# Kernel tuning notes

Hardware: AMD Instinct MI355X
Metric: run time of the kernel (lower is better)

Reference implementation:

```python
import jax, jax.numpy as jnp
import numpy as np

N_NODES = 50000
N_EDGES = 800000
N_REL = 16
N_GRAPHS = 64
IN_DIM = 128
HID = 128
FC = 256
N_CLASSES = 16


def setup_inputs() -> dict:
    key = jax.random.key(0)
    ks = jax.random.split(key, 16)
    h = jax.random.normal(ks[0], (N_NODES, IN_DIM), dtype=jnp.float32)
    src = jax.random.randint(ks[1], (N_EDGES,), 0, N_NODES, dtype=jnp.int32)
    dst = jax.random.randint(ks[2], (N_EDGES,), 0, N_NODES, dtype=jnp.int32)
    rel_types = jax.random.randint(ks[3], (N_EDGES,), 0, N_REL, dtype=jnp.int32)
    graph_ids = jnp.sort(jax.random.randint(ks[4], (N_NODES,), 0, N_GRAPHS, dtype=jnp.int32))
    s1 = 1.0 / np.sqrt(IN_DIM)
    s2 = 1.0 / np.sqrt(HID)
    # RGCN layer 1: per-relation weights, self-loop weight, bias
    W1 = jax.random.normal(ks[5], (N_REL, IN_DIM, HID), dtype=jnp.float32) * s1
    Ws1 = jax.random.normal(ks[6], (IN_DIM, HID), dtype=jnp.float32) * s1
    b1 = jnp.zeros((HID,), dtype=jnp.float32)
    # RGCN layer 2
    W2 = jax.random.normal(ks[7], (N_REL, HID, HID), dtype=jnp.float32) * s2
    Ws2 = jax.random.normal(ks[8], (HID, HID), dtype=jnp.float32) * s2
    b2 = jnp.zeros((HID,), dtype=jnp.float32)
    # FC layer after mean pooling
    Wfc = jax.random.normal(ks[9], (HID, FC), dtype=jnp.float32) * s2
    bfc = jnp.zeros((FC,), dtype=jnp.float32)
    # classify head
    Wc = jax.random.normal(ks[10], (FC, N_CLASSES), dtype=jnp.float32) * (1.0 / np.sqrt(FC))
    bc = jnp.zeros((N_CLASSES,), dtype=jnp.float32)
    return dict(h=h, src=src, dst=dst, rel_types=rel_types, graph_ids=graph_ids,
                W1=W1, Ws1=Ws1, b1=b1, W2=W2, Ws2=Ws2, b2=b2,
                Wfc=Wfc, bfc=bfc, Wc=Wc, bc=bc)


def _rel_graph_conv(h, W, Ws, b, src, dst, rel):
    # dgl RelGraphConv (regularizer=None, self_loop=True, bias=True):
    # out[v] = sum_{e:(u->v)} W[rel_e] @ h[u] + Ws @ h[v] + b
    hW = jnp.einsum('ni,rio->rno', h, W)            # [R, N, out]
    msg = hW[rel, src]                               # [E, out] gather per edge
    agg = jax.ops.segment_sum(msg, dst, num_segments=N_NODES)
    return agg + h @ Ws + b


def _mean_nodes(h, graph_ids):
    sums = jax.ops.segment_sum(h, graph_ids, num_segments=N_GRAPHS)      # [G, D]
    cnts = jax.ops.segment_sum(jnp.ones((h.shape[0], 1), h.dtype), graph_ids,
                               num_segments=N_GRAPHS)                    # [G, 1]
    return sums / jnp.maximum(cnts, 1.0)


def reference(h, src, dst, rel_types, graph_ids,
              W1, Ws1, b1, W2, Ws2, b2, Wfc, bfc, Wc, bc):
    h = h.astype(jnp.float32)
    h = jax.nn.relu(_rel_graph_conv(h, W1, Ws1, b1, src, dst, rel_types))
    h = jax.nn.relu(_rel_graph_conv(h, W2, Ws2, b2, src, dst, rel_types))
    hg = _mean_nodes(h, graph_ids)                   # [G, HID]
    hg = jax.nn.relu(hg @ Wfc + bfc)                 # [G, FC]
    return jax.nn.softmax(hg @ Wc + bc, axis=1)      # [G, n_classes]
```

## Files before the change

### kernel.cpp

```cpp
#include <hip/hip_runtime.h>
#include <hip/hip_bf16.h>

#define N_NODES   50000
#define N_PAD     50048
#define N_EDGES   800000
#define N_REL     16
#define N_GRAPHS  64
#define DIM       128
#define FC_DIM    256
#define N_CLASSES 16

#define SB        50176
#define NBINS_P   (16 * SB)
#define NBLK_PP   784
#define NCOARSE   782
#define NCH       98
#define CHSZ      8192
#define POOL_CH   64
#define NBVIRT    13328

#define WS_MARK   0
#define WS_HG     802816
#define WS_CNT    835584
#define WS_SRCOF  835840
#define MEMSET_SZ 4038912
#define WS_BLKH   4038912
#define WS_COFS   4345600
#define WS_PARTP  4348928
#define WS_BLKB   4352256
#define WS_RELB   4355584
#define WS_CIDMAP 4355840
#define WS_RTMP   7567104
#define WS_RECS   10767104
#define WS_OFFSD  13967104
#define WS_X1     14167552
#define WS_X2     26979840
#define WS_AGG    39792128
#define WS_WB     52604416
#define WS_T      53718528

#define XW_TOTAL  (N_PAD * DIM + 2 * 17 * 16384)

typedef __attribute__((ext_vector_type(8))) short bf16x8;
typedef __attribute__((ext_vector_type(4))) float f32x4;

__device__ __forceinline__ void atomAddF(float* p, float v) {
#if defined(__gfx90a__) || defined(__gfx942__) || defined(__gfx950__)
    unsafeAtomicAdd(p, v);
#else
    atomicAdd(p, v);
#endif
}

__device__ __forceinline__ float bf2f(unsigned int u) {
    union { float f; unsigned int i; } x; x.i = u << 16; return x.f;
}
__device__ __forceinline__ unsigned short f2bf(float f) {
    union { float f; unsigned int u; } x; x.f = f;
    unsigned int r = x.u + 0x7fff + ((x.u >> 16) & 1);
    return (unsigned short)(r >> 16);
}
__device__ __forceinline__ void accum8(float* qa, uint4 u) {
    qa[0] += bf2f(u.x & 0xffff); qa[1] += bf2f(u.x >> 16);
    qa[2] += bf2f(u.y & 0xffff); qa[3] += bf2f(u.y >> 16);
    qa[4] += bf2f(u.z & 0xffff); qa[5] += bf2f(u.z >> 16);
    qa[6] += bf2f(u.w & 0xffff); qa[7] += bf2f(u.w >> 16);
}
__device__ __forceinline__ void pack16(const float* qa, unsigned short* dst) {
    #pragma unroll
    for (int j = 0; j < 2; ++j) {
        uint4 w;
        w.x = ((unsigned int)f2bf(qa[j*8+1]) << 16) | f2bf(qa[j*8+0]);
        w.y = ((unsigned int)f2bf(qa[j*8+3]) << 16) | f2bf(qa[j*8+2]);
        w.z = ((unsigned int)f2bf(qa[j*8+5]) << 16) | f2bf(qa[j*8+4]);
        w.w = ((unsigned int)f2bf(qa[j*8+7]) << 16) | f2bf(qa[j*8+6]);
        ((uint4*)dst)[j] = w;
    }
}

__global__ void k_convXW(const float* __restrict__ h, unsigned short* __restrict__ x1,
                         const float* __restrict__ W1, const float* __restrict__ Ws1,
                         const float* __restrict__ W2, const float* __restrict__ Ws2,
                         unsigned short* __restrict__ Wb) {
    int id = blockIdx.x * blockDim.x + threadIdx.x;
    if (id < N_PAD * DIM) {
        int v = id >> 7;
        x1[id] = (v < N_NODES) ? f2bf(h[id]) : (unsigned short)0;
    } else {
        int t = id - N_PAD * DIM;
        int l = t / 278528, rem = t % 278528;
        int r = rem >> 14, rr = rem & 16383;
        int n = rr >> 7, k = rr & 127;
        const float* W  = l ? W2 : W1;
        const float* Ws = l ? Ws2 : Ws1;
        float v = (r < 16) ? W[r * 16384 + k * 128 + n] : Ws[k * 128 + n];
        Wb[t] = f2bf(v);
    }
}

__global__ __launch_bounds__(256) void k_h1(
    const int* __restrict__ src, const int* __restrict__ dst, const int* __restrict__ rel,
    unsigned char* __restrict__ mark, int* __restrict__ blockHist)
{
    __shared__ int hl[NCOARSE];
    int b = blockIdx.x, t = threadIdx.x;
    for (int i = t; i < NCOARSE; i += 256) hl[i] = 0;
    __syncthreads();
    int e0 = b * CHSZ;
    int eend = min(e0 + CHSZ, N_EDGES);
    for (int e = e0 + t; e < eend; e += 256) {
        int d = dst[e];
        mark[rel[e] * SB + src[e]] = 1;
        atomicAdd(&hl[d >> 6], 1);
    }
    __syncthreads();
    for (int i = t; i < NCOARSE; i += 256) blockHist[b * NCOARSE + i] = hl[i];
}

__global__ void k_cscan(int* __restrict__ blockHist, int* __restrict__ coarseOffs) {
    __shared__ int s1[1024], s2[1024];
    int t = threadIdx.x;
    int tot = 0;
    if (t < NCOARSE) {
        int run = 0;
        for (int b = 0; b < NCH; ++b) {
            int v = blockHist[b * NCOARSE + t];
            blockHist[b * NCOARSE + t] = run;
            run += v;
        }
        tot = run;
    }
    s1[t] = tot; __syncthreads();
    int* cur = s1; int* nxt = s2;
    for (int o = 1; o < 1024; o <<= 1) {
        nxt[t] = cur[t] + ((t >= o) ? cur[t - o] : 0);
        __syncthreads();
        int* tmp = cur; cur = nxt; nxt = tmp;
    }
    if (t < NCOARSE) {
        int base = cur[t] - tot;
        coarseOffs[t] = base;
        for (int b = 0; b < NCH; ++b) blockHist[b * NCOARSE + t] += base;
    }
    if (t == NCOARSE) coarseOffs[NCOARSE] = cur[NCOARSE - 1];
}

__global__ void k_scanPA(const unsigned int* __restrict__ markU, int* __restrict__ partP) {
    __shared__ int red[256];
    int b = blockIdx.x, t = threadIdx.x;
    unsigned int u = markU[b * 256 + t];
    red[t] = (int)((u & 1) + ((u >> 8) & 1) + ((u >> 16) & 1) + ((u >> 24) & 1));
    __syncthreads();
    for (int o = 128; o > 0; o >>= 1) {
        if (t < o) red[t] += red[t + o];
        __syncthreads();
    }
    if (t == 0) partP[b] = red[0];
}

__global__ void k_scanPB(const int* __restrict__ partP, int* __restrict__ blkB,
                         int* __restrict__ relB) {
    __shared__ int s1[784], s2[784];
    __shared__ int tot[16], rbase[17];
    int t = threadIdx.x;
    int rel = t / 49, pos = t - rel * 49;
    int v = (t < 784) ? partP[t] : 0;
    if (t < 784) s1[t] = v;
    __syncthreads();
    int* cur = s1; int* nxt = s2;
    for (int o = 1; o < 64; o <<= 1) {
        if (t < 784) nxt[t] = cur[t] + ((pos >= o) ? cur[t - o] : 0);
        __syncthreads();
        int* tmp = cur; cur = nxt; nxt = tmp;
    }
    if (t < 784 && pos == 48) tot[rel] = cur[t];
    __syncthreads();
    if (t == 0) {
        int base = 0;
        for (int r = 0; r < 16; ++r) { rbase[r] = base; base += (tot[r] + 63) & ~63; }
        rbase[16] = base;
    }
    __syncthreads();
    if (t < 784) blkB[t] = rbase[rel] + cur[t] - v;
    if (t < 17)  relB[t] = rbase[t];
}

__global__ void k_scanPC(const unsigned int* __restrict__ markU, const int* __restrict__ blkB,
                         int* __restrict__ cidMap, int* __restrict__ srcOf) {
    __shared__ int s1[256], s2[256];
    int b = blockIdx.x, t = threadIdx.x;
    unsigned int u = markU[b * 256 + t];
    int f0 = (int)(u & 1), f1 = (int)((u >> 8) & 1);
    int f2 = (int)((u >> 16) & 1), f3 = (int)((u >> 24) & 1);
    int sum = f0 + f1 + f2 + f3;
    s1[t] = sum; __syncthreads();
    int* cur = s1; int* nxt = s2;
    for (int o = 1; o < 256; o <<= 1) {
        nxt[t] = cur[t] + ((t >= o) ? cur[t - o] : 0);
        __syncthreads();
        int* tmp = cur; cur = nxt; nxt = tmp;
    }
    int cid = blkB[b] + cur[t] - sum;
    int rel = b / 49;
    int key0 = b * 1024 + t * 4;
    int srcBase = key0 - rel * SB;
    if (f0) { cidMap[key0]     = cid; srcOf[cid] = srcBase;     cid++; }
    if (f1) { cidMap[key0 + 1] = cid; srcOf[cid] = srcBase + 1; cid++; }
    if (f2) { cidMap[key0 + 2] = cid; srcOf[cid] = srcBase + 2; cid++; }
    if (f3) { cidMap[key0 + 3] = cid; srcOf[cid] = srcBase + 3; cid++; }
}

__global__ __launch_bounds__(256) void k_scat1(
    const int* __restrict__ src, const int* __restrict__ dst, const int* __restrict__ rel,
    const int* __restrict__ cidMap, const int* __restrict__ blockHist,
    unsigned int* __restrict__ rtmp)
{
    __shared__ int baseL[NCOARSE];
    __shared__ int hl[NCOARSE];
    int b = blockIdx.x, t = threadIdx.x;
    for (int i = t; i < NCOARSE; i += 256) { baseL[i] = blockHist[b * NCOARSE + i]; hl[i] = 0; }
    __syncthreads();
    int e0 = b * CHSZ;
    int eend = min(e0 + CHSZ, N_EDGES);
    for (int e = e0 + t; e < eend; e += 256) {
        int d = dst[e];
        int cid = cidMap[rel[e] * SB + src[e]];
        int c = d >> 6;
        int rank = atomicAdd(&hl[c], 1);
        rtmp[baseL[c] + rank] = ((unsigned int)cid << 6) | (unsigned int)(d & 63);
    }
}

__global__ __launch_bounds__(256) void k_p2(
    const unsigned int* __restrict__ rtmp, const int* __restrict__ coarseOffs,
    unsigned int* __restrict__ recs, int* __restrict__ offsD)
{
    __shared__ int cntL[64], exclL[65], cur2[64];
    int i = blockIdx.x, t = threadIdx.x;
    int segB = coarseOffs[i], segE = coarseOffs[i + 1];
    if (t < 64) { cntL[t] = 0; cur2[t] = 0; }
    __syncthreads();
    for (int e = segB + t; e < segE; e += 256)
        atomicAdd(&cntL[rtmp[e] & 63u], 1);
    __syncthreads();
    if (t == 0) {
        int run = segB;
        #pragma unroll
        for (int d = 0; d < 64; ++d) { exclL[d] = run; run += cntL[d]; }
        exclL[64] = run;
    }
    __syncthreads();
    if (t < 64) offsD[i * 64 + t] = exclL[t];
    if (t == 64) offsD[i * 64 + 64] = exclL[64];
    for (int e = segB + t; e < segE; e += 256) {
        unsigned int r = rtmp[e];
        int d = (int)(r & 63u);
        int rank = atomicAdd(&cur2[d], 1);
        recs[exclL[d] + rank] = r >> 6;
    }
}

__global__ __launch_bounds__(256) void k_phaseA(
    const unsigned short* __restrict__ x, const unsigned short* __restrict__ Wb,
    const int* __restrict__ srcOf, const int* __restrict__ relB,
    unsigned short* __restrict__ T)
{
    __shared__ unsigned short Xs[64 * 136];
    __shared__ unsigned short Cs[64 * 136];
    __shared__ int sSrc[64];
    __shared__ int sRB[17];

    int tid = threadIdx.x;
    if (tid < 17) sRB[tid] = relB[tid];
    __syncthreads();
    int rtot = sRB[16];

    for (int vb = blockIdx.x; vb < NBVIRT; vb += gridDim.x) {
        int chunk = vb / 136;
        int lane  = vb - chunk * 136;
        int r = lane >> 3;
        int i = chunk * 8 + (lane & 7);
        int base, cnt;
        if (r == 16) { base = rtot;    cnt = N_PAD / 64; }
        else         { base = sRB[r];  cnt = (sRB[r + 1] - base) >> 6; }
        if (i >= cnt) continue;
        int row0 = base + i * 64;

        __syncthreads();
        if (tid < 64) sSrc[tid] = (r == 16) ? (i * 64 + tid) : srcOf[row0 + tid];
        __syncthreads();

        {
            int row = tid >> 2, c0 = tid & 3;
            const uint4* xp = (const uint4*)(x + (size_t)sSrc[row] * DIM);
            uint4* lp = (uint4*)(&Xs[row * 136]);
            #pragma unroll
            for (int ii = 0; ii < 4; ++ii) lp[c0 + 4 * ii] = xp[c0 + 4 * ii];
        }
        __syncthreads();

        int w = tid >> 6, l = tid & 63;
        int nl = l & 15, q = l >> 4;

        bf16x8 Bf[2][4];
        const unsigned short* wr = Wb + r * 16384;
        #pragma unroll
        for (int nt = 0; nt < 2; ++nt) {
            int n = w * 32 + nt * 16 + nl;
            #pragma unroll
            for (int kc = 0; kc < 4; ++kc)
                Bf[nt][kc] = *(const bf16x8*)(wr + n * 128 + kc * 32 + q * 8);
        }
        #pragma unroll
        for (int m = 0; m < 4; ++m) {
            f32x4 a0 = {0.f,0.f,0.f,0.f}, a1 = {0.f,0.f,0.f,0.f};
            #pragma unroll
            for (int kc = 0; kc < 4; ++kc) {
                bf16x8 a = *(const bf16x8*)(&Xs[(m * 16 + nl) * 136 + kc * 32 + q * 8]);
                a0 = __builtin_amdgcn_mfma_f32_16x16x32_bf16(a, Bf[0][kc], a0, 0, 0, 0);
                a1 = __builtin_amdgcn_mfma_f32_16x16x32_bf16(a, Bf[1][kc], a1, 0, 0, 0);
            }
            int col = w * 32 + nl;
            #pragma unroll
            for (int reg = 0; reg < 4; ++reg) {
                int row = m * 16 + q * 4 + reg;
                Cs[row * 136 + col]      = f2bf(a0[reg]);
                Cs[row * 136 + col + 16] = f2bf(a1[reg]);
            }
        }
        __syncthreads();
        {
            unsigned short* Tb = T + (size_t)row0 * DIM;
            #pragma unroll
            for (int it = 0; it < 4; ++it) {
                int c = tid + it * 256;
                int row = c >> 4, k8 = c & 15;
                uint4 vv = *(const uint4*)(&Cs[row * 136 + k8 * 8]);
                *(uint4*)(Tb + row * DIM + k8 * 8) = vv;
            }
        }
    }
}

__global__ __launch_bounds__(256) void k_phaseB(
    const unsigned short* __restrict__ T, const unsigned int* __restrict__ recs,
    const int* __restrict__ offsD, const int* __restrict__ relB,
    const float* __restrict__ bias,
    unsigned short* __restrict__ aggOut, int relu)
{
    __shared__ int sOffs[33];
    __shared__ float sBias[128];
    __shared__ int sSelf;
    int tid = threadIdx.x;
    int v0 = blockIdx.x * 32;
    if (tid < 33) sOffs[tid] = offsD[v0 + tid];
    if (tid == 40) sSelf = relB[16];
    if (tid >= 64 && tid < 96) ((float4*)sBias)[tid - 64] = ((const float4*)bias)[tid - 64];
    __syncthreads();

    int g = tid >> 3, s = tid & 7;
    int dst = v0 + g;
    float qa[16];
    #pragma unroll
    for (int i = 0; i < 16; ++i) qa[i] = sBias[s * 16 + i];

    int beg = sOffs[g], end = sOffs[g + 1];
    int e = beg;
    for (; e + 3 < end; e += 4) {
        unsigned int c0 = recs[e], c1 = recs[e+1], c2 = recs[e+2], c3 = recs[e+3];
        const uint4* t0 = (const uint4*)(T + (size_t)c0 * DIM + s * 16);
        const uint4* t1 = (const uint4*)(T + (size_t)c1 * DIM + s * 16);
        const uint4* t2 = (const uint4*)(T + (size_t)c2 * DIM + s * 16);
        const uint4* t3 = (const uint4*)(T + (size_t)c3 * DIM + s * 16);
        uint4 a0 = t0[0], a1 = t0[1], b0 = t1[0], b1 = t1[1];
        uint4 cc0 = t2[0], cc1 = t2[1], d0 = t3[0], d1 = t3[1];
        accum8(qa, a0); accum8(qa + 8, a1);
        accum8(qa, b0); accum8(qa + 8, b1);
        accum8(qa, cc0); accum8(qa + 8, cc1);
        accum8(qa, d0); accum8(qa + 8, d1);
    }
    for (; e < end; ++e) {
        unsigned int c = recs[e];
        const uint4* tp = (const uint4*)(T + (size_t)c * DIM + s * 16);
        uint4 u0 = tp[0], u1 = tp[1];
        accum8(qa, u0); accum8(qa + 8, u1);
    }
    {
        const uint4* tp = (const uint4*)(T + (size_t)(sSelf + dst) * DIM + s * 16);
        uint4 u0 = tp[0], u1 = tp[1];
        accum8(qa, u0); accum8(qa + 8, u1);
    }

    if (relu) {
        #pragma unroll
        for (int i = 0; i < 16; ++i) qa[i] = fmaxf(qa[i], 0.f);
    }
    pack16(qa, aggOut + (size_t)dst * DIM + s * 16);
}

__global__ void k_pool(const unsigned short* __restrict__ agg2, const int* __restrict__ gids,
                       float* __restrict__ hg_sum, int* __restrict__ cnt)
{
    int d  = threadIdx.x;
    int n0 = blockIdx.x * POOL_CH;
    int nend = min(n0 + POOL_CH, N_NODES);
    if (n0 >= N_NODES) return;
    int curg = gids[n0];
    float run = 0.f;
    for (int n = n0; n < nend; ++n) {
        int g = gids[n];
        if (g != curg) { atomAddF(&hg_sum[curg*DIM + d], run); run = 0.f; curg = g; }
        run += fmaxf(bf2f((unsigned int)agg2[n*DIM + d]), 0.f);
    }
    atomAddF(&hg_sum[curg*DIM + d], run);
    if (d == 0) {
        int cg = gids[n0]; int rl = 0;
        for (int n = n0; n < nend; ++n) {
            int g = gids[n];
            if (g != cg) { atomicAdd(&cnt[cg], rl); rl = 0; cg = g; }
            rl++;
        }
        atomicAdd(&cnt[cg], rl);
    }
}

__global__ __launch_bounds__(256) void k_head(
    const float* __restrict__ hg_sum, const int* __restrict__ cnt,
    const float* __restrict__ Wfc, const float* __restrict__ bfc,
    const float* __restrict__ Wc, const float* __restrict__ bc,
    float* __restrict__ out)
{
    int g = blockIdx.x, t = threadIdx.x;
    __shared__ float hgl[DIM];
    __shared__ float fcl[FC_DIM];
    __shared__ float lg[N_CLASSES];
    if (t < DIM) {
        float c = (float)max(cnt[g], 1);
        hgl[t] = hg_sum[g*DIM + t] / c;
    }
    __syncthreads();
    {
        float sv = bfc[t];
        #pragma unroll 4
        for (int k = 0; k < DIM; ++k) sv += hgl[k] * Wfc[k*FC_DIM + t];
        fcl[t] = fmaxf(sv, 0.f);
    }
    __syncthreads();
    if (t < N_CLASSES) {
        float lgt = bc[t];
        #pragma unroll 4
        for (int k = 0; k < FC_DIM; ++k) lgt += fcl[k] * Wc[k*N_CLASSES + t];
        lg[t] = lgt;
    }
    __syncthreads();
    if (t < N_CLASSES) {
        float m = lg[0];
        #pragma unroll
        for (int c = 1; c < N_CLASSES; ++c) m = fmaxf(m, lg[c]);
        float sden = 0.f;
        #pragma unroll
        for (int c = 0; c < N_CLASSES; ++c) sden += expf(lg[c] - m);
        out[g*N_CLASSES + t] = expf(lg[t] - m) / sden;
    }
}

extern "C" void kernel_launch(void* const* d_in, const int* in_sizes, int n_in,
                              void* d_out, int out_size, void* d_ws, size_t ws_size,
                              hipStream_t stream)
{
    const float* h   = (const float*)d_in[0];
    const int*   src = (const int*)d_in[1];
    const int*   dst = (const int*)d_in[2];
    const int*   rel = (const int*)d_in[3];
    const int*   gid = (const int*)d_in[4];
    const float* W1  = (const float*)d_in[5];
    const float* Ws1 = (const float*)d_in[6];
    const float* b1  = (const float*)d_in[7];
    const float* W2  = (const float*)d_in[8];
    const float* Ws2 = (const float*)d_in[9];
    const float* b2  = (const float*)d_in[10];
    const float* Wfc = (const float*)d_in[11];
    const float* bfc = (const float*)d_in[12];
    const float* Wc  = (const float*)d_in[13];
    const float* bc  = (const float*)d_in[14];
    float* out = (float*)d_out;

    char* ws = (char*)d_ws;
    unsigned char* mark = (unsigned char*)(ws + WS_MARK);
    float* hgsum = (float*)(ws + WS_HG);
    int*   cnt   = (int*)(ws + WS_CNT);
    int*   srcOf = (int*)(ws + WS_SRCOF);
    int*   blkH  = (int*)(ws + WS_BLKH);
    int*   cOffs = (int*)(ws + WS_COFS);
    int*   partP = (int*)(ws + WS_PARTP);
    int*   blkB  = (int*)(ws + WS_BLKB);
    int*   relB  = (int*)(ws + WS_RELB);
    int*   cidMap= (int*)(ws + WS_CIDMAP);
    unsigned int* rtmp = (unsigned int*)(ws + WS_RTMP);
    unsigned int* recs = (unsigned int*)(ws + WS_RECS);
    int*   offsD = (int*)(ws + WS_OFFSD);
    unsigned short* x1  = (unsigned short*)(ws + WS_X1);
    unsigned short* x2  = (unsigned short*)(ws + WS_X2);
    unsigned short* agg = (unsigned short*)(ws + WS_AGG);
    unsigned short* Wb  = (unsigned short*)(ws + WS_WB);
    unsigned short* T   = (unsigned short*)(ws + WS_T);

    int gridA = NBVIRT;
    if (ws_size > (size_t)WS_T) {
        long long capRows = (long long)((ws_size - WS_T) / 256);
        long long capBlk = capRows / 64;
        if (capBlk < gridA) gridA = (int)capBlk;
    }

    hipMemsetAsync(mark, 0, MEMSET_SZ, stream);

    k_convXW<<<XW_TOTAL / 256, 256, 0, stream>>>(h, x1, W1, Ws1, W2, Ws2, Wb);
    k_h1<<<NCH, 256, 0, stream>>>(src, dst, rel, mark, blkH);

    k_cscan<<<1, 1024, 0, stream>>>(blkH, cOffs);
    k_scanPA<<<NBLK_PP, 256, 0, stream>>>((const unsigned int*)mark, partP);
    k_scanPB<<<1, 1024, 0, stream>>>(partP, blkB, relB);
    k_scanPC<<<NBLK_PP, 256, 0, stream>>>((const unsigned int*)mark, blkB, cidMap, srcOf);

    k_scat1<<<NCH, 256, 0, stream>>>(src, dst, rel, cidMap, blkH, rtmp);
    k_p2<<<NCOARSE, 256, 0, stream>>>(rtmp, cOffs, recs, offsD);

    k_phaseA<<<gridA, 256, 0, stream>>>(x1, Wb, srcOf, relB, T);
    k_phaseB<<<N_PAD / 32, 256, 0, stream>>>(T, recs, offsD, relB, b1, x2, 1);
    k_phaseA<<<gridA, 256, 0, stream>>>(x2, Wb + 17 * 16384, srcOf, relB, T);
    k_phaseB<<<N_PAD / 32, 256, 0, stream>>>(T, recs, offsD, relB, b2, agg, 0);

    k_pool<<<(N_PAD + POOL_CH - 1) / POOL_CH, 128, 0, stream>>>(agg, gid, hgsum, cnt);
    k_head<<<N_GRAPHS, 256, 0, stream>>>(hgsum, cnt, Wfc, bfc, Wc, bc, out);
}
```

Measured before the change: 439.8 us.

## Software-pipeline phaseA gathers with persistent grid and swizzled LDS output

Turns k_phaseA into a persistent kernel with a fixed grid of 1024 blocks. Each block prefetches the next tile's gathered source rows into registers while computing the current tile's MFMA, and no longer stages source indices in shared memory. It also XOR-swizzles the Cs staging buffer to reduce LDS bank conflicts. The intent is to hide gather latency and cut syncs per tile, at the cost of extra registers and dropping the workspace-capacity-based grid limit.

Result: no change. 433.9 us (-1.3%).

```diff
diff --git a/kernel.cpp b/kernel.cpp
--- a/kernel.cpp
+++ b/kernel.cpp
@@ -18,6 +18,7 @@
 #define CHSZ      8192
 #define POOL_CH   64
 #define NBVIRT    13328
+#define GRID_A    1024
 
 #define WS_MARK   0
 #define WS_HG     802816
@@ -265,9 +266,8 @@
     const int* __restrict__ srcOf, const int* __restrict__ relB,
     unsigned short* __restrict__ T)
 {
-    __shared__ unsigned short Xs[64 * 136];
-    __shared__ unsigned short Cs[64 * 136];
-    __shared__ int sSrc[64];
+    __shared__ __attribute__((aligned(16))) unsigned short Xs[64 * 136];
+    __shared__ __attribute__((aligned(16))) unsigned short Cs[64 * 136];
     __shared__ int sRB[17];
 
     int tid = threadIdx.x;
@@ -275,70 +275,94 @@
     __syncthreads();
     int rtot = sRB[16];
 
-    for (int vb = blockIdx.x; vb < NBVIRT; vb += gridDim.x) {
+    int row = tid >> 2, c0 = tid & 3;
+
+    auto tileInfo = [&](int vb, int& trow0, int& tr) -> bool {
         int chunk = vb / 136;
-        int lane  = vb - chunk * 136;
+        int lane = vb - chunk * 136;
         int r = lane >> 3;
         int i = chunk * 8 + (lane & 7);
         int base, cnt;
-        if (r == 16) { base = rtot;    cnt = N_PAD / 64; }
-        else         { base = sRB[r];  cnt = (sRB[r + 1] - base) >> 6; }
-        if (i >= cnt) continue;
-        int row0 = base + i * 64;
-
+        if (r == 16) { base = rtot; cnt = N_PAD / 64; }
+        else         { base = sRB[r]; cnt = (sRB[r + 1] - base) >> 6; }
+        if (i >= cnt) return false;
+        trow0 = base + i * 64; tr = r;
+        return true;
+    };
+
+    int vb = blockIdx.x;
+    int cur_row0, cur_r;
+    while (vb < NBVIRT && !tileInfo(vb, cur_row0, cur_r)) vb += gridDim.x;
+    if (vb >= NBVIRT) return;
+
+    uint4 g0, g1, g2, g3;
+    {
+        int sr = (cur_r == 16) ? (cur_row0 - rtot + row) : srcOf[cur_row0 + row];
+        const uint4* xp = (const uint4*)(x + (size_t)sr * DIM);
+        g0 = xp[c0]; g1 = xp[c0 + 4]; g2 = xp[c0 + 8]; g3 = xp[c0 + 12];
+    }
+
+    int w = tid >> 6, l = tid & 63;
+    int nl = l & 15, q = l >> 4;
+
+    while (true) {
+        {
+            uint4* lp = (uint4*)(&Xs[row * 136]);
+            lp[c0] = g0; lp[c0 + 4] = g1; lp[c0 + 8] = g2; lp[c0 + 12] = g3;
+        }
+        bf16x8 Bf[2][4];
+        {
+            const unsigned short* wr = Wb + cur_r * 16384;
+            #pragma unroll
+            for (int nt = 0; nt < 2; ++nt) {
+                int n = w * 32 + nt * 16 + nl;
+                #pragma unroll
+                for (int kc = 0; kc < 4; ++kc)
+                    Bf[nt][kc] = *(const bf16x8*)(wr + n * 128 + kc * 32 + q * 8);
+            }
+        }
+        int nvb = vb + gridDim.x;
+        int nxt_row0 = 0, nxt_r = 0;
+        while (nvb < NBVIRT && !tileInfo(nvb, nxt_row0, nxt_r)) nvb += gridDim.x;
+        bool nhave = (nvb < NBVIRT);
+        if (nhave) {
+            int sr = (nxt_r == 16) ? (nxt_row0 - rtot + row) : srcOf[nxt_row0 + row];
+            const uint4* xp = (const uint4*)(x + (size_t)sr * DIM);
+            g0 = xp[c0]; g1 = xp[c0 + 4]; g2 = xp[c0 + 8]; g3 = xp[c0 + 12];
+        }
         __syncthreads();
-        if (tid < 64) sSrc[tid] = (r == 16) ? (i * 64 + tid) : srcOf[row0 + tid];
-        __syncthreads();
-
-        {
-            int row = tid >> 2, c0 = tid & 3;
-            const uint4* xp = (const uint4*)(x + (size_t)sSrc[row] * DIM);
-            uint4* lp = (uint4*)(&Xs[row * 136]);
-            #pragma unroll
-            for (int ii = 0; ii < 4; ++ii) lp[c0 + 4 * ii] = xp[c0 + 4 * ii];
-        }
-        __syncthreads();
-
-        int w = tid >> 6, l = tid & 63;
-        int nl = l & 15, q = l >> 4;
-
-        bf16x8 Bf[2][4];
-        const unsigned short* wr = Wb + r * 16384;
-        #pragma unroll
-        for (int nt = 0; nt < 2; ++nt) {
-            int n = w * 32 + nt * 16 + nl;
-            #pragma unroll
-            for (int kc = 0; kc < 4; ++kc)
-                Bf[nt][kc] = *(const bf16x8*)(wr + n * 128 + kc * 32 + q * 8);
-        }
         #pragma unroll
         for (int m = 0; m < 4; ++m) {
-            f32x4 a0 = {0.f,0.f,0.f,0.f}, a1 = {0.f,0.f,0.f,0.f};
+            f32x4 a0 = {0.f, 0.f, 0.f, 0.f}, a1 = {0.f, 0.f, 0.f, 0.f};
             #pragma unroll
             for (int kc = 0; kc < 4; ++kc) {
                 bf16x8 a = *(const bf16x8*)(&Xs[(m * 16 + nl) * 136 + kc * 32 + q * 8]);
                 a0 = __builtin_amdgcn_mfma_f32_16x16x32_bf16(a, Bf[0][kc], a0, 0, 0, 0);
                 a1 = __builtin_amdgcn_mfma_f32_16x16x32_bf16(a, Bf[1][kc], a1, 0, 0, 0);
             }
-            int col = w * 32 + nl;
+            int colb = w * 32 + nl;
             #pragma unroll
             for (int reg = 0; reg < 4; ++reg) {
-                int row = m * 16 + q * 4 + reg;
-                Cs[row * 136 + col]      = f2bf(a0[reg]);
-                Cs[row * 136 + col + 16] = f2bf(a1[reg]);
+                int row2 = m * 16 + q * 4 + reg;
+                int sw = ((row2 >> 3) & 1) << 4;
+                Cs[row2 * 136 + (colb ^ sw)]        = f2bf(a0[reg]);
+                Cs[row2 * 136 + ((colb + 16) ^ sw)] = f2bf(a1[reg]);
             }
         }
         __syncthreads();
         {
-            unsigned short* Tb = T + (size_t)row0 * DIM;
+            unsigned short* Tb = T + (size_t)cur_row0 * DIM;
             #pragma unroll
             for (int it = 0; it < 4; ++it) {
                 int c = tid + it * 256;
-                int row = c >> 4, k8 = c & 15;
-                uint4 vv = *(const uint4*)(&Cs[row * 136 + k8 * 8]);
-                *(uint4*)(Tb + row * DIM + k8 * 8) = vv;
+                int rw = c >> 4, k8 = c & 15;
+                int sw = ((rw >> 3) & 1) << 4;
+                uint4 vv = *(const uint4*)(&Cs[rw * 136 + ((k8 * 8) ^ sw)]);
+                *(uint4*)(Tb + rw * DIM + k8 * 8) = vv;
             }
         }
+        if (!nhave) break;
+        vb = nvb; cur_row0 = nxt_row0; cur_r = nxt_r;
     }
 }
 
@@ -505,13 +529,6 @@
     unsigned short* Wb  = (unsigned short*)(ws + WS_WB);
     unsigned short* T   = (unsigned short*)(ws + WS_T);
 
-    int gridA = NBVIRT;
-    if (ws_size > (size_t)WS_T) {
-        long long capRows = (long long)((ws_size - WS_T) / 256);
-        long long capBlk = capRows / 64;
-        if (capBlk < gridA) gridA = (int)capBlk;
-    }
-
     hipMemsetAsync(mark, 0, MEMSET_SZ, stream);
 
     k_convXW<<<XW_TOTAL / 256, 256, 0, stream>>>(h, x1, W1, Ws1, W2, Ws2, Wb);
@@ -525,9 +542,9 @@
     k_scat1<<<NCH, 256, 0, stream>>>(src, dst, rel, cidMap, blkH, rtmp);
     k_p2<<<NCOARSE, 256, 0, stream>>>(rtmp, cOffs, recs, offsD);
 
-    k_phaseA<<<gridA, 256, 0, stream>>>(x1, Wb, srcOf, relB, T);
+    k_phaseA<<<GRID_A, 256, 0, stream>>>(x1, Wb, srcOf, relB, T);
     k_phaseB<<<N_PAD / 32, 256, 0, stream>>>(T, recs, offsD, relB, b1, x2, 1);
-    k_phaseA<<<gridA, 256, 0, stream>>>(x2, Wb + 17 * 16384, srcOf, relB, T);
+    k_phaseA<<<GRID_A, 256, 0, stream>>>(x2, Wb + 17 * 16384, srcOf, relB, T);
     k_phaseB<<<N_PAD / 32, 256, 0, stream>>>(T, recs, offsD, relB, b2, agg, 0);
 
     k_pool<<<(N_PAD + POOL_CH - 1) / POOL_CH, 128, 0, stream>>>(agg, gid, hgsum, cnt);
```
